# Kernel tuning notes

Hardware: AMD Instinct MI355X
Metric: run time of the kernel (lower is better)

The kernel has to match this reference:

```python
import jax, jax.numpy as jnp
import numpy as np

N = 8192
D_IN = 32
HIDDEN = [32, 32, 32]   # -> 2 GraphConvolution layers
FC = [32, 1]            # hfc = [32, 32, 1] -> 2 Linear layers


def _uniform(key, shape, stdv):
    return jax.random.uniform(key, shape, jnp.float32, -stdv, stdv)


def setup_inputs() -> dict:
    key = jax.random.key(0)
    ks = jax.random.split(key, 32)
    inp = {}
    inp["V"] = jax.random.normal(ks[0], (N, D_IN), jnp.float32)
    inp["adj"] = jax.random.randint(ks[1], (N, N), 0, 4, jnp.int32)
    # GCN layer params: w1, w2, w3 [in, out], bias [out]; init U(-stdv, stdv), stdv = 1/sqrt(out)
    ki = 2
    for li in range(len(HIDDEN) - 1):
        a, b = HIDDEN[li], HIDDEN[li + 1]
        stdv = 1.0 / np.sqrt(b)
        for wname in ("w1", "w2", "w3"):
            inp[f"{wname}_{li}"] = _uniform(ks[ki], (a, b), stdv); ki += 1
        inp[f"gb_{li}"] = _uniform(ks[ki], (b,), stdv); ki += 1
    # FC params (torch Linear default init: U(-1/sqrt(in), 1/sqrt(in)))
    hfc = [HIDDEN[-1]] + FC
    for li in range(len(hfc) - 1):
        a, b = hfc[li], hfc[li + 1]
        stdv = 1.0 / np.sqrt(a)
        inp[f"fcW_{li}"] = _uniform(ks[ki], (b, a), stdv); ki += 1  # torch Linear weight is [out, in]
        inp[f"fcb_{li}"] = _uniform(ks[ki], (b,), stdv); ki += 1
    return inp


def _gcn(V, adj, w1, w2, w3, bias):
    # masked-adjacency relational aggregation: sum_k (adj==k) @ (V @ w_k)
    dt = V.dtype
    o = (adj == 1).astype(dt) @ (V @ w1)
    o = o + (adj == 2).astype(dt) @ (V @ w2)
    o = o + (adj == 3).astype(dt) @ (V @ w3)
    return jax.nn.relu(o + bias)


def reference(V, adj, w1_0, w2_0, w3_0, gb_0, w1_1, w2_1, w3_1, gb_1,
              fcW_0, fcb_0, fcW_1, fcb_1):
    Z = _gcn(V, adj, w1_0, w2_0, w3_0, gb_0)          # [N, 32]
    Z = _gcn(Z, adj, w1_1, w2_1, w3_1, gb_1)          # [N, 32]
    Z = jnp.sum(Z, axis=0)                             # [32] sum pooling over nodes
    Z = jax.nn.relu(Z @ fcW_0.T + fcb_0)               # dropout = identity (eval mode)
    Z = Z @ fcW_1.T + fcb_1                            # [1]
    return jax.nn.sigmoid(Z)
```

## Files before the change

### kernel.cpp

```cpp
#include <hip/hip_runtime.h>
#include <cmath>

#define NN 8192

typedef float floatx4 __attribute__((ext_vector_type(4)));
typedef unsigned int uint;
typedef unsigned long long u64;

__global__ __launch_bounds__(256) void h_kernel(
    const float* __restrict__ X, const float* __restrict__ w1,
    const float* __restrict__ w2, const float* __restrict__ w3,
    u64* __restrict__ Hfrag) {
  __shared__ float wl[32][32];
  __shared__ float Xs[64][32];
  const int tid = threadIdx.x;
  const int ch = blockIdx.y;
  const float* wsrc = (ch == 0) ? w1 : (ch == 1) ? w2 : w3;
  for (int i = tid; i < 1024; i += 256) ((float*)wl)[i] = wsrc[i];
  const size_t base = (size_t)blockIdx.x * 2048 + tid * 8;
  float4 x0 = ((const float4*)(X + base))[0];
  float4 x1 = ((const float4*)(X + base))[1];
  *((float4*)(&Xs[0][0] + tid * 8)) = x0;
  *((float4*)(&Xs[0][0] + tid * 8 + 4)) = x1;
  __syncthreads();
  const int n = tid & 31, jb = tid >> 5;
  const int j0 = blockIdx.x * 64 + jb * 8;
  const int t = j0 >> 5;
  const int lane = (n & 15) | (((j0 & 31) >> 3) << 4);
  const int tile = n >> 4;
  float av[8];
#pragma unroll
  for (int jj = 0; jj < 8; ++jj) {
    const float4* xr = (const float4*)(&Xs[jb * 8 + jj][0]);
    float acc = 0.f;
#pragma unroll
    for (int d4 = 0; d4 < 8; ++d4) {
      float4 x = xr[d4];
      acc += x.x * wl[d4 * 4 + 0][n];
      acc += x.y * wl[d4 * 4 + 1][n];
      acc += x.z * wl[d4 * 4 + 2][n];
      acc += x.w * wl[d4 * 4 + 3][n];
    }
    av[jj] = acc;
  }
  int lo = __builtin_amdgcn_cvt_pk_fp8_f32(av[0], av[1], 0, false);
  lo = __builtin_amdgcn_cvt_pk_fp8_f32(av[2], av[3], lo, true);
  int hi = __builtin_amdgcn_cvt_pk_fp8_f32(av[4], av[5], 0, false);
  hi = __builtin_amdgcn_cvt_pk_fp8_f32(av[6], av[7], hi, true);
  size_t idx = (((size_t)ch * 256 + t) * 2 + tile) * 64 + lane;
  Hfrag[idx] = ((u64)(uint)hi << 32) | (uint)(uint)lo;
}

#define BUILD_MASK(z, r0out, r1out)                                       \
  {                                                                       \
    const uint d0 = ((((z) & 0x55u) * 0x41041u) & 0x01010101u) << 6;      \
    const uint d1 = (((((z) >> 8) & 0x55u) * 0x41041u) & 0x01010101u)     \
                    << 6;                                                 \
    const uint d2 = (((((z) >> 16) & 0x55u) * 0x41041u) & 0x01010101u)    \
                    << 6;                                                 \
    const uint d3 = (((((z) >> 24) & 0x55u) * 0x41041u) & 0x01010101u)    \
                    << 6;                                                 \
    r0out = (long long)(((u64)d1 << 32) | d0);                            \
    r1out = (long long)(((u64)d3 << 32) | d2);                            \
  }

#define MF8(A, B, C) __builtin_amdgcn_mfma_f32_16x16x32_fp8_fp8((A), (B), (C), 0, 0, 0)

__device__ __forceinline__ void phaseB4(uint4 mkv, const u64* __restrict__ hp,
                                        floatx4& acc00, floatx4& acc01,
                                        floatx4& acc10, floatx4& acc11) {
  uint mk[4] = {mkv.x, mkv.y, mkv.z, mkv.w};
  long long b00 = (long long)hp[0],     b01 = (long long)hp[64];
  long long b10 = (long long)hp[32768], b11 = (long long)hp[32768 + 64];
  long long b20 = (long long)hp[65536], b21 = (long long)hp[65536 + 64];
#pragma unroll
  for (int tl = 0; tl < 4; ++tl) {
    long long n00, n01, n10, n11, n20, n21;
    if (tl < 3) {
      const u64* np = hp + (tl + 1) * 128;
      n00 = (long long)np[0];     n01 = (long long)np[64];
      n10 = (long long)np[32768]; n11 = (long long)np[32768 + 64];
      n20 = (long long)np[65536]; n21 = (long long)np[65536 + 64];
    }
    const uint pk = mk[tl];
    const uint x1 = pk ^ 0x55555555u;
    const uint z1 = ~(x1 | (x1 >> 1)) & 0x55555555u;
    const uint x2 = pk ^ 0xAAAAAAAAu;
    const uint z2 = ~(x2 | (x2 >> 1)) & 0x55555555u;
    const uint x3 = ~pk;
    const uint z3 = ~(x3 | (x3 >> 1)) & 0x55555555u;
    long long a1r0, a1r1, a2r0, a2r1, a3r0, a3r1;
    BUILD_MASK(z1, a1r0, a1r1);
    BUILD_MASK(z2, a2r0, a2r1);
    BUILD_MASK(z3, a3r0, a3r1);
    acc00 = MF8(a1r0, b00, acc00);
    acc00 = MF8(a2r0, b10, acc00);
    acc00 = MF8(a3r0, b20, acc00);
    acc01 = MF8(a1r0, b01, acc01);
    acc01 = MF8(a2r0, b11, acc01);
    acc01 = MF8(a3r0, b21, acc01);
    acc10 = MF8(a1r1, b00, acc10);
    acc10 = MF8(a2r1, b10, acc10);
    acc10 = MF8(a3r1, b20, acc10);
    acc11 = MF8(a1r1, b01, acc11);
    acc11 = MF8(a2r1, b11, acc11);
    acc11 = MF8(a3r1, b21, acc11);
    if (tl < 3) {
      b00 = n00; b01 = n01; b10 = n10; b11 = n11; b20 = n20; b21 = n21;
    }
  }
}

__global__ __launch_bounds__(512, 2) void agg1_kernel(
    const int* __restrict__ adj, uint* __restrict__ packed_g,
    const u64* __restrict__ Hf1, u64* __restrict__ Hf2,
    const float* __restrict__ w1, const float* __restrict__ w2,
    const float* __restrict__ w3, const float* __restrict__ gb0) {
  __shared__ __align__(16) char smraw[65536];
  uint* pt0 = (uint*)smraw;
  uint* pt1 = (uint*)(smraw + 8192);
  float (*red)[4][64][4] = (float (*)[4][64][4])(smraw + 16384);
  float* wl = (float*)(smraw + 49152);
  float* Zs = (float*)smraw;
  const int tid = threadIdx.x;
  const int rg = blockIdx.x;
  const int w = tid >> 6, lane = tid & 63;
  for (int i = tid; i < 3072; i += 512) {
    const int chw = i >> 10;
    const float* wsrc = (chw == 0) ? w1 : (chw == 1) ? w2 : w3;
    wl[i] = wsrc[i & 1023];
  }
  const int tid2 = tid & 255, rhalf = tid >> 8;
  const int byte_base = (tid2 >> 5) * 1024 + ((tid2 >> 1) & 3) * 256 +
                        ((tid2 >> 3) & 3) * 4 + (tid2 & 1);
  const int* abase =
      adj + (size_t)rg * 32 * NN + (size_t)rhalf * 16 * NN + tid2 * 4;
  {
    int4 a[16];
#pragma unroll
    for (int rr = 0; rr < 16; ++rr)
      a[rr] = *(const int4*)(abase + (size_t)rr * NN);
    unsigned char* pb = (unsigned char*)pt0;
#pragma unroll
    for (int rr = 0; rr < 16; ++rr) {
      const int r = rhalf * 16 + rr;
      const uint b = (uint)(a[rr].x & 3) | ((uint)(a[rr].y & 3) << 2) |
                     ((uint)(a[rr].z & 3) << 4) | ((uint)(a[rr].w & 3) << 6);
      pb[byte_base + (r & 15) * 16 + (r >> 4) * 2] = (unsigned char)b;
    }
  }
  __syncthreads();
  floatx4 acc00 = {0.f, 0.f, 0.f, 0.f}, acc01 = {0.f, 0.f, 0.f, 0.f};
  floatx4 acc10 = {0.f, 0.f, 0.f, 0.f}, acc11 = {0.f, 0.f, 0.f, 0.f};
  for (int c = 0; c < 8; ++c) {
    uint* ptc = (c & 1) ? pt1 : pt0;
    uint* ptn = (c & 1) ? pt0 : pt1;
    int4 a[16];
    if (c < 7) {
#pragma unroll
      for (int rr = 0; rr < 16; ++rr)
        a[rr] = *(const int4*)(abase + (c + 1) * 1024 + (size_t)rr * NN);
    }
    uint* pg = packed_g + ((size_t)rg * 8 + c) * 2048;
    *(uint4*)(pg + tid * 4) = *(const uint4*)(ptc + tid * 4);
    const uint4 mkv = *(const uint4*)(ptc + w * 256 + lane * 4);
    const u64* hp = Hf1 + (size_t)(c * 32 + w * 4) * 128 + lane;
    phaseB4(mkv, hp, acc00, acc01, acc10, acc11);
    if (c < 7) {
      unsigned char* pb = (unsigned char*)ptn;
#pragma unroll
      for (int rr = 0; rr < 16; ++rr) {
        const int r = rhalf * 16 + rr;
        const uint b = (uint)(a[rr].x & 3) | ((uint)(a[rr].y & 3) << 2) |
                       ((uint)(a[rr].z & 3) << 4) | ((uint)(a[rr].w & 3) << 6);
        pb[byte_base + (r & 15) * 16 + (r >> 4) * 2] = (unsigned char)b;
      }
    }
    __syncthreads();
  }
#pragma unroll
  for (int r = 0; r < 4; ++r) {
    red[w][0][lane][r] = acc00[r];
    red[w][1][lane][r] = acc01[r];
    red[w][2][lane][r] = acc10[r];
    red[w][3][lane][r] = acc11[r];
  }
  __syncthreads();
  if (w == 0) {
    const int m = lane & 15, q = lane >> 4;
#pragma unroll
    for (int r = 0; r < 4; ++r) {
      float c00 = 0.f, c01 = 0.f, c10 = 0.f, c11 = 0.f;
#pragma unroll
      for (int i = 0; i < 8; ++i) {
        c00 += red[i][0][lane][r];
        c01 += red[i][1][lane][r];
        c10 += red[i][2][lane][r];
        c11 += red[i][3][lane][r];
      }
      const int ro = q * 4 + r;
      float z00 = 0.5f * c00 + gb0[m];
      float z01 = 0.5f * c01 + gb0[16 + m];
      float z10 = 0.5f * c10 + gb0[m];
      float z11 = 0.5f * c11 + gb0[16 + m];
      z00 = z00 > 0.f ? z00 : 0.f;
      z01 = z01 > 0.f ? z01 : 0.f;
      z10 = z10 > 0.f ? z10 : 0.f;
      z11 = z11 > 0.f ? z11 : 0.f;
      Zs[ro * 33 + m] = z00;
      Zs[ro * 33 + 16 + m] = z01;
      Zs[(ro + 16) * 33 + m] = z10;
      Zs[(ro + 16) * 33 + 16 + m] = z11;
    }
  }
  __syncthreads();
  if (tid < 384) {
    const int chp = tid >> 7, rem = tid & 127;
    const int tile = rem >> 6, l2 = rem & 63;
    const int n = tile * 16 + (l2 & 15), j0 = (l2 >> 4) * 8;
    const float* wc = wl + chp * 1024;
    float av[8];
#pragma unroll
    for (int e = 0; e < 8; ++e) {
      float acc = 0.f;
      const float* zr = Zs + (j0 + e) * 33;
#pragma unroll
      for (int d = 0; d < 32; ++d) acc += zr[d] * wc[d * 32 + n];
      av[e] = acc;
    }
    int lo = __builtin_amdgcn_cvt_pk_fp8_f32(av[0], av[1], 0, false);
    lo = __builtin_amdgcn_cvt_pk_fp8_f32(av[2], av[3], lo, true);
    int hi = __builtin_amdgcn_cvt_pk_fp8_f32(av[4], av[5], 0, false);
    hi = __builtin_amdgcn_cvt_pk_fp8_f32(av[6], av[7], hi, true);
    Hf2[(((size_t)chp * 256 + rg) * 2 + tile) * 64 + l2] =
        ((u64)(uint)hi << 32) | (uint)(uint)lo;
  }
}

__global__ __launch_bounds__(512, 2) void agg2_kernel(
    const uint* __restrict__ packed_g, const u64* __restrict__ Hf2,
    const float* __restrict__ gb1, float* __restrict__ partials) {
  __shared__ float red[8][4][64][4];
  const int tid = threadIdx.x;
  const int rg = blockIdx.x;
  const int w = tid >> 6, lane = tid & 63;
  floatx4 acc00 = {0.f, 0.f, 0.f, 0.f}, acc01 = {0.f, 0.f, 0.f, 0.f};
  floatx4 acc10 = {0.f, 0.f, 0.f, 0.f}, acc11 = {0.f, 0.f, 0.f, 0.f};
  const uint* pgb = packed_g + (size_t)rg * 8 * 2048 + w * 256 + lane * 4;
  for (int c = 0; c < 8; ++c) {
    const uint4 mkv = *(const uint4*)(pgb + c * 2048);
    const u64* hp = Hf2 + (size_t)(c * 32 + w * 4) * 128 + lane;
    phaseB4(mkv, hp, acc00, acc01, acc10, acc11);
  }
#pragma unroll
  for (int r = 0; r < 4; ++r) {
    red[w][0][lane][r] = acc00[r];
    red[w][1][lane][r] = acc01[r];
    red[w][2][lane][r] = acc10[r];
    red[w][3][lane][r] = acc11[r];
  }
  __syncthreads();
  if (w == 0) {
    const int m = lane & 15;
    float s0 = 0.f, s1 = 0.f;
#pragma unroll
    for (int r = 0; r < 4; ++r) {
      float c00 = 0.f, c01 = 0.f, c10 = 0.f, c11 = 0.f;
#pragma unroll
      for (int i = 0; i < 8; ++i) {
        c00 += red[i][0][lane][r];
        c01 += red[i][1][lane][r];
        c10 += red[i][2][lane][r];
        c11 += red[i][3][lane][r];
      }
      float z00 = 0.5f * c00 + gb1[m];
      float z01 = 0.5f * c01 + gb1[16 + m];
      float z10 = 0.5f * c10 + gb1[m];
      float z11 = 0.5f * c11 + gb1[16 + m];
      s0 += (z00 > 0.f ? z00 : 0.f) + (z10 > 0.f ? z10 : 0.f);
      s1 += (z01 > 0.f ? z01 : 0.f) + (z11 > 0.f ? z11 : 0.f);
    }
    s0 += __shfl_xor(s0, 16);
    s0 += __shfl_xor(s0, 32);
    s1 += __shfl_xor(s1, 16);
    s1 += __shfl_xor(s1, 32);
    if ((lane >> 4) == 0) {
      partials[rg * 32 + m] = s0;
      partials[rg * 32 + 16 + m] = s1;
    }
  }
}

__global__ __launch_bounds__(256) void fc_kernel(
    const float* __restrict__ partials, int np, const float* __restrict__ W0,
    const float* __restrict__ b0, const float* __restrict__ W1,
    const float* __restrict__ b1, float* __restrict__ out) {
  __shared__ float acc8[8][32];
  __shared__ float z[32], y[32];
  const int tid = threadIdx.x;
  const int col = tid & 31, ch = tid >> 5;
  float s = 0.f;
  for (int i = ch; i < np; i += 8) s += partials[(size_t)i * 32 + col];
  acc8[ch][col] = s;
  __syncthreads();
  if (tid < 32) {
    float t = 0.f;
#pragma unroll
    for (int i = 0; i < 8; ++i) t += acc8[i][tid];
    z[tid] = t;
  }
  __syncthreads();
  if (tid < 32) {
    float acc = b0[tid];
    for (int n = 0; n < 32; ++n) acc += W0[tid * 32 + n] * z[n];
    y[tid] = acc > 0.f ? acc : 0.f;
  }
  __syncthreads();
  if (tid == 0) {
    float acc = b1[0];
    for (int mm = 0; mm < 32; ++mm) acc += W1[mm] * y[mm];
    out[0] = 1.f / (1.f + expf(-acc));
  }
}

extern "C" void kernel_launch(void* const* d_in, const int* in_sizes, int n_in,
                              void* d_out, int out_size, void* d_ws,
                              size_t ws_size, hipStream_t stream) {
  const float* V   = (const float*)d_in[0];
  const int*   adj = (const int*)d_in[1];
  const float *w10 = (const float*)d_in[2], *w20 = (const float*)d_in[3],
              *w30 = (const float*)d_in[4], *gb0 = (const float*)d_in[5];
  const float *w11 = (const float*)d_in[6], *w21 = (const float*)d_in[7],
              *w31 = (const float*)d_in[8], *gb1 = (const float*)d_in[9];
  const float *fW0 = (const float*)d_in[10], *fb0 = (const float*)d_in[11],
              *fW1 = (const float*)d_in[12], *fb1 = (const float*)d_in[13];
  float* out = (float*)d_out;
  char* ws = (char*)d_ws;

  u64*   Hf1      = (u64*)ws;
  u64*   Hf2      = (u64*)(ws + 786432);
  uint*  packed   = (uint*)(ws + 1572864);
  float* partials = (float*)(ws + 18350080);

  h_kernel<<<dim3(128, 3), 256, 0, stream>>>(V, w10, w20, w30, Hf1);
  agg1_kernel<<<256, 512, 0, stream>>>(adj, packed, Hf1, Hf2, w11, w21, w31,
                                       gb0);
  agg2_kernel<<<256, 512, 0, stream>>>(packed, Hf2, gb1, partials);
  fc_kernel<<<1, 256, 0, stream>>>(partials, 256, fW0, fb0, fW1, fb1, out);
}
```

Measured before the change: 411.2 us.

## Fuse FC head into agg2 via last-block atomics; prefetch H fragments in agg1

```diff
diff --git a/kernel.cpp b/kernel.cpp
--- a/kernel.cpp
+++ b/kernel.cpp
@@ -10,11 +10,16 @@
 __global__ __launch_bounds__(256) void h_kernel(
     const float* __restrict__ X, const float* __restrict__ w1,
     const float* __restrict__ w2, const float* __restrict__ w3,
-    u64* __restrict__ Hfrag) {
+    u64* __restrict__ Hfrag, float* __restrict__ accg,
+    uint* __restrict__ cnt) {
   __shared__ float wl[32][32];
   __shared__ float Xs[64][32];
   const int tid = threadIdx.x;
   const int ch = blockIdx.y;
+  if (blockIdx.x == 0 && ch == 0) {
+    if (tid < 32) accg[tid] = 0.f;
+    if (tid == 32) *cnt = 0u;
+  }
   const float* wsrc = (ch == 0) ? w1 : (ch == 1) ? w2 : w3;
   for (int i = tid; i < 1024; i += 256) ((float*)wl)[i] = wsrc[i];
   const size_t base = (size_t)blockIdx.x * 2048 + tid * 8;
@@ -64,7 +69,37 @@
     r1out = (long long)(((u64)d3 << 32) | d2);                            \
   }
 
+#define ZCH(pk, K, zout)                                                  \
+  {                                                                       \
+    const uint x_ = (pk) ^ (K);                                           \
+    zout = ~(x_ | (x_ >> 1)) & 0x55555555u;                               \
+  }
+
 #define MF8(A, B, C) __builtin_amdgcn_mfma_f32_16x16x32_fp8_fp8((A), (B), (C), 0, 0, 0)
+
+#define TILE_MFMA(pk, B00, B01, B10, B11, B20, B21)                       \
+  {                                                                       \
+    uint z1_, z2_, z3_;                                                   \
+    ZCH(pk, 0x55555555u, z1_);                                            \
+    ZCH(pk, 0xAAAAAAAAu, z2_);                                            \
+    ZCH(pk, 0xFFFFFFFFu, z3_);                                            \
+    long long a1r0, a1r1, a2r0, a2r1, a3r0, a3r1;                         \
+    BUILD_MASK(z1_, a1r0, a1r1);                                          \
+    BUILD_MASK(z2_, a2r0, a2r1);                                          \
+    BUILD_MASK(z3_, a3r0, a3r1);                                          \
+    acc00 = MF8(a1r0, B00, acc00);                                        \
+    acc00 = MF8(a2r0, B10, acc00);                                        \
+    acc00 = MF8(a3r0, B20, acc00);                                        \
+    acc01 = MF8(a1r0, B01, acc01);                                        \
+    acc01 = MF8(a2r0, B11, acc01);                                        \
+    acc01 = MF8(a3r0, B21, acc01);                                        \
+    acc10 = MF8(a1r1, B00, acc10);                                        \
+    acc10 = MF8(a2r1, B10, acc10);                                        \
+    acc10 = MF8(a3r1, B20, acc10);                                        \
+    acc11 = MF8(a1r1, B01, acc11);                                        \
+    acc11 = MF8(a2r1, B11, acc11);                                        \
+    acc11 = MF8(a3r1, B21, acc11);                                        \
+  }
 
 __device__ __forceinline__ void phaseB4(uint4 mkv, const u64* __restrict__ hp,
                                         floatx4& acc00, floatx4& acc01,
@@ -83,35 +118,14 @@
       n20 = (long long)np[65536]; n21 = (long long)np[65536 + 64];
     }
     const uint pk = mk[tl];
-    const uint x1 = pk ^ 0x55555555u;
-    const uint z1 = ~(x1 | (x1 >> 1)) & 0x55555555u;
-    const uint x2 = pk ^ 0xAAAAAAAAu;
-    const uint z2 = ~(x2 | (x2 >> 1)) & 0x55555555u;
-    const uint x3 = ~pk;
-    const uint z3 = ~(x3 | (x3 >> 1)) & 0x55555555u;
-    long long a1r0, a1r1, a2r0, a2r1, a3r0, a3r1;
-    BUILD_MASK(z1, a1r0, a1r1);
-    BUILD_MASK(z2, a2r0, a2r1);
-    BUILD_MASK(z3, a3r0, a3r1);
-    acc00 = MF8(a1r0, b00, acc00);
-    acc00 = MF8(a2r0, b10, acc00);
-    acc00 = MF8(a3r0, b20, acc00);
-    acc01 = MF8(a1r0, b01, acc01);
-    acc01 = MF8(a2r0, b11, acc01);
-    acc01 = MF8(a3r0, b21, acc01);
-    acc10 = MF8(a1r1, b00, acc10);
-    acc10 = MF8(a2r1, b10, acc10);
-    acc10 = MF8(a3r1, b20, acc10);
-    acc11 = MF8(a1r1, b01, acc11);
-    acc11 = MF8(a2r1, b11, acc11);
-    acc11 = MF8(a3r1, b21, acc11);
+    TILE_MFMA(pk, b00, b01, b10, b11, b20, b21);
     if (tl < 3) {
       b00 = n00; b01 = n01; b10 = n10; b11 = n11; b20 = n20; b21 = n21;
     }
   }
 }
 
-__global__ __launch_bounds__(512, 2) void agg1_kernel(
+__global__ __launch_bounds__(512, 1) void agg1_kernel(
     const int* __restrict__ adj, uint* __restrict__ packed_g,
     const u64* __restrict__ Hf1, u64* __restrict__ Hf2,
     const float* __restrict__ w1, const float* __restrict__ w2,
@@ -155,6 +169,23 @@
   for (int c = 0; c < 8; ++c) {
     uint* ptc = (c & 1) ? pt1 : pt0;
     uint* ptn = (c & 1) ? pt0 : pt1;
+    const u64* hp = Hf1 + (size_t)(c * 32 + w * 4) * 128 + lane;
+    long long bf0[6], bf1[6], bf2[6], bf3[6];
+#pragma unroll
+    for (int f = 0; f < 1; ++f) {
+      bf0[0] = (long long)hp[0];       bf0[1] = (long long)hp[64];
+      bf0[2] = (long long)hp[32768];   bf0[3] = (long long)hp[32768 + 64];
+      bf0[4] = (long long)hp[65536];   bf0[5] = (long long)hp[65536 + 64];
+      bf1[0] = (long long)hp[128];     bf1[1] = (long long)hp[128 + 64];
+      bf1[2] = (long long)hp[32896];   bf1[3] = (long long)hp[32896 + 64];
+      bf1[4] = (long long)hp[65664];   bf1[5] = (long long)hp[65664 + 64];
+      bf2[0] = (long long)hp[256];     bf2[1] = (long long)hp[256 + 64];
+      bf2[2] = (long long)hp[33024];   bf2[3] = (long long)hp[33024 + 64];
+      bf2[4] = (long long)hp[65792];   bf2[5] = (long long)hp[65792 + 64];
+      bf3[0] = (long long)hp[384];     bf3[1] = (long long)hp[384 + 64];
+      bf3[2] = (long long)hp[33152];   bf3[3] = (long long)hp[33152 + 64];
+      bf3[4] = (long long)hp[65920];   bf3[5] = (long long)hp[65920 + 64];
+    }
     int4 a[16];
     if (c < 7) {
 #pragma unroll
@@ -164,8 +195,10 @@
     uint* pg = packed_g + ((size_t)rg * 8 + c) * 2048;
     *(uint4*)(pg + tid * 4) = *(const uint4*)(ptc + tid * 4);
     const uint4 mkv = *(const uint4*)(ptc + w * 256 + lane * 4);
-    const u64* hp = Hf1 + (size_t)(c * 32 + w * 4) * 128 + lane;
-    phaseB4(mkv, hp, acc00, acc01, acc10, acc11);
+    TILE_MFMA(mkv.x, bf0[0], bf0[1], bf0[2], bf0[3], bf0[4], bf0[5]);
+    TILE_MFMA(mkv.y, bf1[0], bf1[1], bf1[2], bf1[3], bf1[4], bf1[5]);
+    TILE_MFMA(mkv.z, bf2[0], bf2[1], bf2[2], bf2[3], bf2[4], bf2[5]);
+    TILE_MFMA(mkv.w, bf3[0], bf3[1], bf3[2], bf3[3], bf3[4], bf3[5]);
     if (c < 7) {
       unsigned char* pb = (unsigned char*)ptn;
 #pragma unroll
@@ -237,10 +270,15 @@
   }
 }
 
-__global__ __launch_bounds__(512, 2) void agg2_kernel(
+__global__ __launch_bounds__(512, 1) void agg2_kernel(
     const uint* __restrict__ packed_g, const u64* __restrict__ Hf2,
-    const float* __restrict__ gb1, float* __restrict__ partials) {
+    const float* __restrict__ gb1, float* __restrict__ accg,
+    uint* __restrict__ cnt, const float* __restrict__ W0,
+    const float* __restrict__ b0, const float* __restrict__ W1,
+    const float* __restrict__ b1, float* __restrict__ out) {
   __shared__ float red[8][4][64][4];
+  __shared__ float fz[32], fy[32];
+  __shared__ uint lastFlag;
   const int tid = threadIdx.x;
   const int rg = blockIdx.x;
   const int w = tid >> 6, lane = tid & 63;
@@ -285,41 +323,30 @@
     s1 += __shfl_xor(s1, 16);
     s1 += __shfl_xor(s1, 32);
     if ((lane >> 4) == 0) {
-      partials[rg * 32 + m] = s0;
-      partials[rg * 32 + 16 + m] = s1;
-    }
-  }
-}
-
-__global__ __launch_bounds__(256) void fc_kernel(
-    const float* __restrict__ partials, int np, const float* __restrict__ W0,
-    const float* __restrict__ b0, const float* __restrict__ W1,
-    const float* __restrict__ b1, float* __restrict__ out) {
-  __shared__ float acc8[8][32];
-  __shared__ float z[32], y[32];
-  const int tid = threadIdx.x;
-  const int col = tid & 31, ch = tid >> 5;
-  float s = 0.f;
-  for (int i = ch; i < np; i += 8) s += partials[(size_t)i * 32 + col];
-  acc8[ch][col] = s;
-  __syncthreads();
-  if (tid < 32) {
-    float t = 0.f;
-#pragma unroll
-    for (int i = 0; i < 8; ++i) t += acc8[i][tid];
-    z[tid] = t;
-  }
-  __syncthreads();
-  if (tid < 32) {
-    float acc = b0[tid];
-    for (int n = 0; n < 32; ++n) acc += W0[tid * 32 + n] * z[n];
-    y[tid] = acc > 0.f ? acc : 0.f;
-  }
-  __syncthreads();
-  if (tid == 0) {
-    float acc = b1[0];
-    for (int mm = 0; mm < 32; ++mm) acc += W1[mm] * y[mm];
-    out[0] = 1.f / (1.f + expf(-acc));
+      atomicAdd(accg + m, s0);
+      atomicAdd(accg + 16 + m, s1);
+    }
+  }
+  __threadfence();
+  __syncthreads();
+  if (tid == 0) lastFlag = (atomicAdd(cnt, 1u) == 255u) ? 1u : 0u;
+  __syncthreads();
+  if (lastFlag) {
+    if (tid < 32) fz[tid] = atomicAdd(accg + tid, 0.f);
+    __syncthreads();
+    if (tid < 32) {
+      float acc = b0[tid];
+#pragma unroll
+      for (int n = 0; n < 32; ++n) acc += W0[tid * 32 + n] * fz[n];
+      fy[tid] = acc > 0.f ? acc : 0.f;
+    }
+    __syncthreads();
+    if (tid == 0) {
+      float acc = b1[0];
+#pragma unroll
+      for (int mm = 0; mm < 32; ++mm) acc += W1[mm] * fy[mm];
+      out[0] = 1.f / (1.f + expf(-acc));
+    }
   }
 }
 
@@ -337,14 +364,16 @@
   float* out = (float*)d_out;
   char* ws = (char*)d_ws;
 
-  u64*   Hf1      = (u64*)ws;
-  u64*   Hf2      = (u64*)(ws + 786432);
-  uint*  packed   = (uint*)(ws + 1572864);
-  float* partials = (float*)(ws + 18350080);
-
-  h_kernel<<<dim3(128, 3), 256, 0, stream>>>(V, w10, w20, w30, Hf1);
+  u64*   Hf1    = (u64*)ws;
+  u64*   Hf2    = (u64*)(ws + 786432);
+  uint*  packed = (uint*)(ws + 1572864);
+  float* accg   = (float*)(ws + 18350080);
+  uint*  cnt    = (uint*)(ws + 18350208);
+
+  h_kernel<<<dim3(128, 3), 256, 0, stream>>>(V, w10, w20, w30, Hf1, accg,
+                                             cnt);
   agg1_kernel<<<256, 512, 0, stream>>>(adj, packed, Hf1, Hf2, w11, w21, w31,
                                        gb0);
-  agg2_kernel<<<256, 512, 0, stream>>>(packed, Hf2, gb1, partials);
-  fc_kernel<<<1, 256, 0, stream>>>(partials, 256, fW0, fb0, fW1, fb1, out);
-}
+  agg2_kernel<<<256, 512, 0, stream>>>(packed, Hf2, gb1, accg, cnt, fW0, fb0,
+                                       fW1, fb1, out);
+}
```

Result: slower. 433.5 us (+5.4%).
